# Performance work log

Hardware: AMD Instinct MI355X
Metric: run time of the kernel (lower is better)

The kernel has to match this reference:

```python
import jax, jax.numpy as jnp
import numpy as np

S = 197      # 'attention_heads' arg, acts as sequence length
D = 768      # embedding_dim
H = 4 * D    # MLP hidden
B = 64
EPS = 1e-5
SCALE = 1.0 / S ** (-0.5)  # faithful to source: equals sqrt(S)


def _ln(x, w, b):
    # LayerNorm over the last two dims (S, D), elementwise affine (S, D)
    mu = jnp.mean(x, axis=(-2, -1), keepdims=True)
    var = jnp.var(x, axis=(-2, -1), keepdims=True)
    return (x - mu) * jax.lax.rsqrt(var + EPS) * w + b


def setup_inputs() -> dict:
    key = jax.random.key(0)
    ks = jax.random.split(key, 16)
    s = 0.02
    return {
        "x": jax.random.normal(ks[0], (B, S, D), jnp.float32),
        "norm1_w": jnp.ones((S, D), jnp.float32),
        "norm1_b": jnp.zeros((S, D), jnp.float32),
        "Wq": jax.random.normal(ks[1], (D, D), jnp.float32) * s,
        "bq": jnp.zeros((D,), jnp.float32),
        "Wk": jax.random.normal(ks[2], (D, D), jnp.float32) * s,
        "bk": jnp.zeros((D,), jnp.float32),
        "Wv": jax.random.normal(ks[3], (D, D), jnp.float32) * s,
        "bv": jnp.zeros((D,), jnp.float32),
        "norm2_w": jnp.ones((S, D), jnp.float32),
        "norm2_b": jnp.zeros((S, D), jnp.float32),
        "W1": jax.random.normal(ks[4], (D, H), jnp.float32) * s,
        "b1": jnp.zeros((H,), jnp.float32),
        "W2": jax.random.normal(ks[5], (H, D), jnp.float32) * s,
        "b2": jnp.zeros((D,), jnp.float32),
    }


def reference(x, norm1_w, norm1_b, Wq, bq, Wk, bk, Wv, bv,
              norm2_w, norm2_b, W1, b1, W2, b2):
    # --- attention block ---
    h = _ln(x, norm1_w, norm1_b)                     # (B, S, D)
    q = jnp.einsum('bsd,de->bse', h, Wq) + bq
    k = jnp.einsum('bsd,de->bse', h, Wk) + bk
    v = jnp.einsum('bsd,de->bse', h, Wv) + bv
    scores = jnp.einsum('bsd,btd->bst', q, k) * SCALE  # (B, S, S)
    attn = jnp.einsum('bst,btd->bsd', jax.nn.softmax(scores, axis=-1), v)
    x = attn + x
    # --- MLP block ---
    h2 = _ln(x, norm2_w, norm2_b)
    hid = jax.nn.gelu(jnp.einsum('bsd,dh->bsh', h2, W1) + b1, approximate=False)
    mlp = jax.nn.gelu(jnp.einsum('bsh,hd->bsd', hid, W2) + b2, approximate=False)
    return mlp + x
```

## Files before the change

### kernel.cpp

```cpp
#include <hip/hip_runtime.h>
#include <math.h>


#define S_LEN 197
#define DIM   768
#define HDIM  3072
#define BATCH 64
#define NT    (BATCH * S_LEN)
#define NTP   12672
#define SD    (S_LEN * DIM)
#define SROWS 208
#define SCOLS 224
#define PROWS 256

typedef __attribute__((ext_vector_type(4))) float  f32x4;
typedef __attribute__((ext_vector_type(8))) short  short8v;
typedef __attribute__((ext_vector_type(4))) short  short4v;
typedef __attribute__((ext_vector_type(4))) unsigned short ushort4v;

__device__ __forceinline__ ushort f2bf(float f) {
  union { float f; unsigned u; } a; a.f = f;
  unsigned u = a.u;
  u += 0x7FFFu + ((u >> 16) & 1u);
  return (ushort)(u >> 16);
}
__device__ __forceinline__ float b2f(ushort h) {
  union { unsigned u; float f; } a; a.u = ((unsigned)h) << 16;
  return a.f;
}
__device__ __forceinline__ float gelu_f(float x) {
  return 0.5f * x * (1.0f + erff(x * 0.7071067811865476f));
}
__device__ __forceinline__ void gload16(const void* g, void* l) {
  __builtin_amdgcn_global_load_lds(
      (const __attribute__((address_space(1))) void*)g,
      (__attribute__((address_space(3))) void*)l, 16, 0, 0);
}

template<bool SPLIT>
__global__ __launch_bounds__(256) void transp_k(const float* __restrict__ W,
                                                int K, int N,
                                                ushort* __restrict__ Thi,
                                                ushort* __restrict__ Tlo) {
  __shared__ float tile[32][33];
  const int nb = blockIdx.x * 32, kb = blockIdx.y * 32;
  const int tx = threadIdx.x, ty = threadIdx.y;
#pragma unroll
  for (int i = 0; i < 4; ++i)
    tile[ty + i * 8][tx] = W[(size_t)(kb + ty + i * 8) * N + nb + tx];
  __syncthreads();
#pragma unroll
  for (int i = 0; i < 4; ++i) {
    float v = tile[tx][ty + i * 8];
    size_t o = (size_t)(nb + ty + i * 8) * K + kb + tx;
    ushort h = f2bf(v);
    Thi[o] = h;
    if (SPLIT) Tlo[o] = f2bf(v - b2f(h));
  }
}

#define LN_CH 4
__global__ __launch_bounds__(256) void ln_part_k(const float* __restrict__ x,
                                                 float* __restrict__ pbuf) {
  const int c = blockIdx.x, b = blockIdx.y;
  const float4* xv = (const float4*)(x + (size_t)b * SD);
  const int per = (SD / 4) / LN_CH;
  float sum = 0.f, sq = 0.f;
  for (int i = c * per + threadIdx.x; i < (c + 1) * per; i += 256) {
    float4 v = xv[i];
    sum += (v.x + v.y) + (v.z + v.w);
    sq  += (v.x * v.x + v.y * v.y) + (v.z * v.z + v.w * v.w);
  }
#pragma unroll
  for (int o = 32; o > 0; o >>= 1) {
    sum += __shfl_xor(sum, o); sq += __shfl_xor(sq, o);
  }
  __shared__ float s1[4], s2[4];
  if ((threadIdx.x & 63) == 0) { s1[threadIdx.x >> 6] = sum; s2[threadIdx.x >> 6] = sq; }
  __syncthreads();
  if (threadIdx.x == 0) {
    pbuf[(b * LN_CH + c) * 2]     = s1[0] + s1[1] + s1[2] + s1[3];
    pbuf[(b * LN_CH + c) * 2 + 1] = s2[0] + s2[1] + s2[2] + s2[3];
  }
}

__global__ __launch_bounds__(64) void ln_fin_k(const float* __restrict__ pbuf,
                                               float* __restrict__ stats) {
  const int b = threadIdx.x;
  float S = 0.f, Q = 0.f;
#pragma unroll
  for (int c = 0; c < LN_CH; ++c) {
    S += pbuf[(b * LN_CH + c) * 2];
    Q += pbuf[(b * LN_CH + c) * 2 + 1];
  }
  const float mu = S / (float)SD;
  const float var = Q / (float)SD - mu * mu;
  stats[b * 2] = mu;
  stats[b * 2 + 1] = 1.0f / sqrtf(var + 1e-5f);
}

template<bool SPLIT>
__global__ __launch_bounds__(256) void ln_apply_k(const float* __restrict__ x,
                                                  const float* __restrict__ w,
                                                  const float* __restrict__ bb,
                                                  const float* __restrict__ stats,
                                                  ushort* __restrict__ oHi,
                                                  ushort* __restrict__ oLo) {
  const int b = blockIdx.y;
  const int i = blockIdx.x * 256 + threadIdx.x;
  if (i >= SD / 4) return;
  const float mu = stats[b * 2], rs = stats[b * 2 + 1];
  float4 v  = ((const float4*)(x + (size_t)b * SD))[i];
  float4 W4 = ((const float4*)w)[i];
  float4 B4 = ((const float4*)bb)[i];
  float h0 = (v.x - mu) * rs * W4.x + B4.x;
  float h1 = (v.y - mu) * rs * W4.y + B4.y;
  float h2 = (v.z - mu) * rs * W4.z + B4.z;
  float h3 = (v.w - mu) * rs * W4.w + B4.w;
  ushort4v hh;
  hh[0] = f2bf(h0); hh[1] = f2bf(h1); hh[2] = f2bf(h2); hh[3] = f2bf(h3);
  ((ushort4v*)(oHi + (size_t)b * SD))[i] = hh;
  if (SPLIT) {
    ushort4v ll;
    ll[0] = f2bf(h0 - b2f(hh[0]));
    ll[1] = f2bf(h1 - b2f(hh[1]));
    ll[2] = f2bf(h2 - b2f(hh[2]));
    ll[3] = f2bf(h3 - b2f(hh[3]));
    ((ushort4v*)(oLo + (size_t)b * SD))[i] = ll;
  }
}

__global__ __launch_bounds__(64) void softmax_k(const float* __restrict__ scores,
                                                ushort* __restrict__ P) {
  const int s = blockIdx.x, b = blockIdx.y;
  const int lane = threadIdx.x;
  const float* row = scores + ((size_t)b * SROWS + s) * SCOLS;
  float v[4];
  float m = -1e30f;
#pragma unroll
  for (int t = 0; t < 4; ++t) {
    int c = lane + t * 64;
    v[t] = (c < S_LEN) ? row[c] : -1e30f;
    m = fmaxf(m, v[t]);
  }
#pragma unroll
  for (int off = 32; off > 0; off >>= 1) m = fmaxf(m, __shfl_xor(m, off));
  float sum = 0.f;
#pragma unroll
  for (int t = 0; t < 4; ++t) {
    int c = lane + t * 64;
    v[t] = (c < S_LEN) ? expf(v[t] - m) : 0.f;
    sum += v[t];
  }
#pragma unroll
  for (int off = 32; off > 0; off >>= 1) sum += __shfl_xor(sum, off);
  const float inv = 1.0f / sum;
  ushort* prow = P + ((size_t)b * PROWS + s) * SCOLS;
#pragma unroll
  for (int t = 0; t < 4; ++t) {
    int c = lane + t * 64;
    if (c < SCOLS) prow[c] = f2bf(v[t] * inv);
  }
}

#define GBM 128
#define GBN 128

enum { EPI_QK = 0, EPI_V, EPI_SCORE, EPI_PV, EPI_GELU, EPI_OUT };

struct GemmArgs {
  const ushort* Ahi; const ushort* Alo; size_t sAb; int lda;
  const ushort* Bhi; const ushort* Blo; size_t sBb; int ldb;
  int K; int Mv; int Nv;
  const float* bias;
  const float* resid; size_t sRb; int ldr;
  float scale;
  float* outF; size_t sOb; int ldo;
  ushort* outHi; ushort* outLo;
};

template<int BK>
__device__ __forceinline__ short8v frag_ld(const ushort* tile, int row, int cb) {
  constexpr int SMASK = (BK * 2) / 16 - 1;
  const char* base = (const char*)tile + row * (BK * 2);
  const int xr = (row & SMASK) << 4;
  const int c1 = cb + 32;
  union U { short8v v8; struct P4 { short4v a, b; } p4; } f;
  f.p4.a = *(const short4v*)(base + ((( cb & ~15) ^ xr) | (cb & 15)));
  f.p4.b = *(const short4v*)(base + (((c1 & ~15) ^ xr) | (c1 & 15)));
  return f.v8;
}

__device__ __forceinline__ short8v load_frag(const ushort* p) {
  union U { short8v v8; struct P4 { short4v a, b; } p4; } f;
  f.p4.a = *(const short4v*)(p);
  f.p4.b = *(const short4v*)(p + 16);
  return f.v8;
}

template<int NPROD, bool TRANSB, int EPI, int BK>
__global__ __launch_bounds__(256) void gemm_k(GemmArgs g) {
  constexpr int KSH2 = (BK == 64) ? 7 : 6;
  constexpr int SMASK = (BK * 2) / 16 - 1;
  constexpr int ASZ  = GBM * BK;
  constexpr int BSTR = TRANSB ? 44 : BK;
  constexpr int BSZ  = GBN * BSTR;
  __shared__ __align__(16) ushort sm[(NPROD == 3) ? (2 * ASZ + 2 * BSZ)
                                                  : (ASZ + BSZ)];
  ushort* sAhi = sm;
  ushort* sBhi = sm + ASZ;
  ushort* sAlo = sm + ASZ + BSZ;
  ushort* sBlo = sm + 2 * ASZ + BSZ;

  const int tid  = threadIdx.x;
  const int lane = tid & 63;
  const int wid  = tid >> 6;
  const int r    = lane & 15;
  const int gg   = lane >> 4;
  const int wrow = wid >> 1;
  const int wcol = wid & 1;

  const int gx = gridDim.x, gy = gridDim.y;
  const int nwg = gx * gy;
  const int orig = blockIdx.x + gx * blockIdx.y;
  const int qq = nwg >> 3, rr = nwg & 7;
  const int xcd = orig & 7, idx = orig >> 3;
  const int wg = (xcd < rr ? xcd * (qq + 1) : rr * (qq + 1) + (xcd - rr) * qq) + idx;
  const int nbase = (wg % gx) * GBN;
  const int mbase = (wg / gx) * GBM;
  const int b     = blockIdx.z;

  const ushort* Ahi = g.Ahi + (size_t)b * g.sAb;
  const ushort* Bhi = g.Bhi + (size_t)b * g.sBb;
  const ushort* Alo = (NPROD == 3) ? (g.Alo + (size_t)b * g.sAb) : (const ushort*)nullptr;
  const ushort* Blo = (NPROD == 3) ? (g.Blo + (size_t)b * g.sBb) : (const ushort*)nullptr;

  f32x4 acc[4][4];
#pragma unroll
  for (int i = 0; i < 4; ++i)
#pragma unroll
    for (int j = 0; j < 4; ++j) {
      acc[i][j][0] = 0.f; acc[i][j][1] = 0.f; acc[i][j][2] = 0.f; acc[i][j][3] = 0.f;
    }

  const int wvb = wid << 10;

  for (int kk = 0; kk < g.K; kk += BK) {
    __syncthreads();
#pragma unroll
    for (int rd = 0; rd < BK / 16; ++rd) {
      const int boff = rd * 4096 + tid * 16;
      const int row  = boff >> KSH2;
      const int slot = (boff >> 4) & SMASK;
      const int scol = ((slot ^ (row & SMASK)) << 3);
      const size_t gaoff = (size_t)(mbase + row) * g.lda + (kk + scol);
      gload16(Ahi + gaoff, (char*)sAhi + rd * 4096 + wvb);
      if (NPROD == 3)
        gload16(Alo + gaoff, (char*)sAlo + rd * 4096 + wvb);
      if (!TRANSB) {
        const size_t gboff = (size_t)(nbase + row) * g.ldb + (kk + scol);
        gload16(Bhi + gboff, (char*)sBhi + rd * 4096 + wvb);
        if (NPROD == 3)
          gload16(Blo + gboff, (char*)sBlo + rd * 4096 + wvb);
      }
    }
    if (TRANSB) {
#pragma unroll
      for (int rd = 0; rd < (BK * 128) / 2048; ++rd) {
        const int lin = tid * 8 + rd * 2048;
        const int kr = lin >> 7, nc = lin & 127;
        union { short8v v; ushort u[8]; } t;
        t.v = *(const short8v*)(Bhi + (size_t)(kk + kr) * g.ldb + (nbase + nc));
#pragma unroll
        for (int e = 0; e < 8; ++e)
          sBhi[(nc + e) * BSTR + kr] = t.u[e];
      }
    }
    __syncthreads();

#pragma unroll
    for (int kb = 0; kb < BK / 32; ++kb) {
      const int cbk = kb * 64 + gg * 8;
      short8v aH[4], bH[4], aL[4], bL[4];
#pragma unroll
      for (int i = 0; i < 4; ++i) {
        const int arow = wrow * 64 + i * 16 + r;
        aH[i] = frag_ld<BK>(sAhi, arow, cbk);
        if (NPROD == 3) aL[i] = frag_ld<BK>(sAlo, arow, cbk);
      }
#pragma unroll
      for (int j = 0; j < 4; ++j) {
        const int brow = wcol * 64 + j * 16 + r;
        if (!TRANSB) {
          bH[j] = frag_ld<BK>(sBhi, brow, cbk);
          if (NPROD == 3) bL[j] = frag_ld<BK>(sBlo, brow, cbk);
        } else {
          bH[j] = load_frag(sBhi + brow * BSTR + kb * 32 + gg * 4);
        }
      }
#pragma unroll
      for (int i = 0; i < 4; ++i)
#pragma unroll
        for (int j = 0; j < 4; ++j) {
          acc[i][j] = __builtin_amdgcn_mfma_f32_16x16x32_bf16(aH[i], bH[j], acc[i][j], 0, 0, 0);
          if (NPROD == 3) {
            acc[i][j] = __builtin_amdgcn_mfma_f32_16x16x32_bf16(aH[i], bL[j], acc[i][j], 0, 0, 0);
            acc[i][j] = __builtin_amdgcn_mfma_f32_16x16x32_bf16(aL[i], bH[j], acc[i][j], 0, 0, 0);
          }
        }
    }
  }

#pragma unroll
  for (int i = 0; i < 4; ++i)
#pragma unroll
    for (int j = 0; j < 4; ++j)
#pragma unroll
      for (int e = 0; e < 4; ++e) {
        const int row = mbase + wrow * 64 + i * 16 + gg * 4 + e;
        const int col = nbase + wcol * 64 + j * 16 + r;
        float val = acc[i][j][e];
        if (EPI == EPI_QK) {
          val += g.bias[col];
          ushort hi = f2bf(val);
          ushort lo = f2bf(val - b2f(hi));
          size_t o = (size_t)row * g.ldo + col;
          g.outHi[o] = hi; g.outLo[o] = lo;
        } else if (EPI == EPI_V) {
          val += g.bias[col];
          g.outHi[(size_t)row * g.ldo + col] = f2bf(val);
        } else if (EPI == EPI_SCORE) {
          if (row < g.Mv && col < g.Nv)
            (g.outF + (size_t)b * g.sOb)[(size_t)row * g.ldo + col] = val * g.scale;
        } else if (EPI == EPI_PV) {
          if (row < g.Mv) {
            val += (g.resid + (size_t)b * g.sRb)[(size_t)row * g.ldr + col];
            (g.outF + (size_t)b * g.sOb)[(size_t)row * g.ldo + col] = val;
          }
        } else if (EPI == EPI_GELU) {
          val = gelu_f(val + g.bias[col]);
          g.outHi[(size_t)row * g.ldo + col] = f2bf(val);
        } else {
          if (row < g.Mv) {
            val = gelu_f(val + g.bias[col]);
            val += g.resid[(size_t)row * g.ldr + col];
            g.outF[(size_t)row * g.ldo + col] = val;
          }
        }
      }
}

extern "C" void kernel_launch(void* const* d_in, const int* in_sizes, int n_in,
                              void* d_out, int out_size, void* d_ws, size_t ws_size,
                              hipStream_t stream) {
  const float* x   = (const float*)d_in[0];
  const float* n1w = (const float*)d_in[1];
  const float* n1b = (const float*)d_in[2];
  const float* Wq  = (const float*)d_in[3];
  const float* bq  = (const float*)d_in[4];
  const float* Wk  = (const float*)d_in[5];
  const float* bk  = (const float*)d_in[6];
  const float* Wv  = (const float*)d_in[7];
  const float* bv  = (const float*)d_in[8];
  const float* n2w = (const float*)d_in[9];
  const float* n2b = (const float*)d_in[10];
  const float* W1  = (const float*)d_in[11];
  const float* b1  = (const float*)d_in[12];
  const float* W2  = (const float*)d_in[13];
  const float* b2  = (const float*)d_in[14];
  float* out = (float*)d_out;

  char* ws = (char*)d_ws;
  size_t off = 0;
  auto alloc = [&](size_t bytes) -> char* {
    char* p = ws + off;
    off += (bytes + 255) & ~(size_t)255;
    return p;
  };
  const size_t szDD  = (size_t)DIM * DIM * 2;
  const size_t szDH  = (size_t)DIM * HDIM * 2;
  const size_t szAct = (size_t)NTP * DIM * 2;

  ushort* wqtH = (ushort*)alloc(szDD);
  ushort* wqtL = (ushort*)alloc(szDD);
  ushort* wktH = (ushort*)alloc(szDD);
  ushort* wktL = (ushort*)alloc(szDD);
  ushort* wvtH = (ushort*)alloc(szDD);
  ushort* w1tH = (ushort*)alloc(szDH);
  ushort* w2tH = (ushort*)alloc(szDH);
  ushort* hHi  = (ushort*)alloc(szAct);
  ushort* hLo  = (ushort*)alloc(szAct);
  ushort* qHi  = (ushort*)alloc(szAct);
  ushort* qLo  = (ushort*)alloc(szAct);
  ushort* kHi  = (ushort*)alloc(szAct);
  ushort* kLo  = (ushort*)alloc(szAct);
  ushort* vB   = (ushort*)alloc(szAct);
  float*  scoresWs = (float*)alloc((size_t)BATCH * SROWS * SCOLS * 4);
  ushort* pWs      = (ushort*)alloc((size_t)BATCH * PROWS * SCOLS * 2);
  float*  lnPart   = (float*)alloc((size_t)BATCH * LN_CH * 2 * 4);
  float*  lnStats  = (float*)alloc((size_t)BATCH * 2 * 4);
  if (off > ws_size) return;

  float*  x2  = (float*)hHi;
  ushort* h2  = vB;
  ushort* hid = qHi;

  const float SCALE_F = 14.035668847618199f;

  dim3 tb(32, 8);
  hipLaunchKernelGGL((transp_k<true >), dim3(DIM / 32, DIM / 32), tb, 0, stream, Wq, DIM, DIM, wqtH, wqtL);
  hipLaunchKernelGGL((transp_k<true >), dim3(DIM / 32, DIM / 32), tb, 0, stream, Wk, DIM, DIM, wktH, wktL);
  hipLaunchKernelGGL((transp_k<false>), dim3(DIM / 32, DIM / 32), tb, 0, stream, Wv, DIM, DIM, wvtH, (ushort*)nullptr);
  hipLaunchKernelGGL((transp_k<false>), dim3(HDIM / 32, DIM / 32), tb, 0, stream, W1, DIM, HDIM, w1tH, (ushort*)nullptr);
  hipLaunchKernelGGL((transp_k<false>), dim3(DIM / 32, HDIM / 32), tb, 0, stream, W2, HDIM, DIM, w2tH, (ushort*)nullptr);

  const int APPLY_BX = (SD / 4 + 255) / 256;
  hipLaunchKernelGGL(ln_part_k, dim3(LN_CH, BATCH), dim3(256), 0, stream, x, lnPart);
  hipLaunchKernelGGL(ln_fin_k, dim3(1), dim3(64), 0, stream, lnPart, lnStats);
  hipLaunchKernelGGL((ln_apply_k<true>), dim3(APPLY_BX, BATCH), dim3(256), 0, stream,
                     x, n1w, n1b, lnStats, hHi, hLo);

  GemmArgs a;
  const int BIG = 0x40000000;

  a = GemmArgs{};
  a.Ahi = hHi; a.Alo = hLo; a.sAb = 0; a.lda = DIM;
  a.Bhi = wqtH; a.Blo = wqtL; a.sBb = 0; a.ldb = DIM;
  a.K = DIM; a.Mv = BIG; a.Nv = BIG; a.bias = bq; a.scale = 1.f;
  a.outHi = qHi; a.outLo = qLo; a.ldo = DIM;
  hipLaunchKernelGGL((gemm_k<3, false, EPI_QK, 32>), dim3(DIM / GBN, NTP / GBM, 1), dim3(256), 0, stream, a);
  a.Bhi = wktH; a.Blo = wktL; a.bias = bk; a.outHi = kHi; a.outLo = kLo;
  hipLaunchKernelGGL((gemm_k<3, false, EPI_QK, 32>), dim3(DIM / GBN, NTP / GBM, 1), dim3(256), 0, stream, a);
  a = GemmArgs{};
  a.Ahi = hHi; a.sAb = 0; a.lda = DIM;
  a.Bhi = wvtH; a.sBb = 0; a.ldb = DIM;
  a.K = DIM; a.Mv = BIG; a.Nv = BIG; a.bias = bv;
  a.outHi = vB; a.ldo = DIM;
  hipLaunchKernelGGL((gemm_k<1, false, EPI_V, 64>), dim3(DIM / GBN, NTP / GBM, 1), dim3(256), 0, stream, a);

  a = GemmArgs{};
  a.Ahi = qHi; a.Alo = qLo; a.sAb = (size_t)SD; a.lda = DIM;
  a.Bhi = kHi; a.Blo = kLo; a.sBb = (size_t)SD; a.ldb = DIM;
  a.K = DIM; a.Mv = S_LEN; a.Nv = S_LEN; a.scale = SCALE_F;
  a.outF = scoresWs; a.sOb = (size_t)SROWS * SCOLS; a.ldo = SCOLS;
  hipLaunchKernelGGL((gemm_k<3, false, EPI_SCORE, 32>), dim3(2, 2, BATCH), dim3(256), 0, stream, a);

  hipLaunchKernelGGL(softmax_k, dim3(S_LEN, BATCH), dim3(64), 0, stream, scoresWs, pWs);

  a = GemmArgs{};
  a.Ahi = pWs; a.sAb = (size_t)PROWS * SCOLS; a.lda = SCOLS;
  a.Bhi = vB; a.sBb = (size_t)SD; a.ldb = DIM;
  a.K = SCOLS; a.Mv = S_LEN; a.Nv = BIG;
  a.resid = x; a.sRb = (size_t)SD; a.ldr = DIM;
  a.outF = x2; a.sOb = (size_t)SD; a.ldo = DIM;
  hipLaunchKernelGGL((gemm_k<1, true, EPI_PV, 32>), dim3(DIM / GBN, 2, BATCH), dim3(256), 0, stream, a);

  hipLaunchKernelGGL(ln_part_k, dim3(LN_CH, BATCH), dim3(256), 0, stream, x2, lnPart);
  hipLaunchKernelGGL(ln_fin_k, dim3(1), dim3(64), 0, stream, lnPart, lnStats);
  hipLaunchKernelGGL((ln_apply_k<false>), dim3(APPLY_BX, BATCH), dim3(256), 0, stream,
                     x2, n2w, n2b, lnStats, h2, (ushort*)nullptr);

  a = GemmArgs{};
  a.Ahi = h2; a.sAb = 0; a.lda = DIM;
  a.Bhi = w1tH; a.sBb = 0; a.ldb = DIM;
  a.K = DIM; a.Mv = BIG; a.Nv = BIG; a.bias = b1;
  a.outHi = hid; a.ldo = HDIM;
  hipLaunchKernelGGL((gemm_k<1, false, EPI_GELU, 64>), dim3(HDIM / GBN, NTP / GBM, 1), dim3(256), 0, stream, a);

  a = GemmArgs{};
  a.Ahi = hid; a.sAb = 0; a.lda = HDIM;
  a.Bhi = w2tH; a.sBb = 0; a.ldb = HDIM;
  a.K = HDIM; a.Mv = NT; a.Nv = BIG; a.bias = b2;
  a.resid = x2; a.sRb = 0; a.ldr = DIM;
  a.outF = out; a.sOb = 0; a.ldo = DIM;
  hipLaunchKernelGGL((gemm_k<1, false, EPI_OUT, 64>), dim3(DIM / GBN, NTP / GBM, 1), dim3(256), 0, stream, a);
}
```

Before: 937.2 us.

## Double-buffer GEMM LDS staging and switch GELU to tanh approximation

For non-transposed-B GEMMs, the shared memory tile becomes double-buffered so the async global-to-LDS loads for the next K step are issued before computing on the current one, with one barrier per iteration. This is meant to overlap memory latency with MFMA work, at the cost of twice the LDS footprint and possibly lower occupancy. Separately, the exact erf GELU is replaced by the tanh approximation built on __expf. That removes the cost of erff but departs from the reference, which requires exact GELU (approximate=False).

```diff
diff --git a/kernel.cpp b/kernel.cpp
--- a/kernel.cpp
+++ b/kernel.cpp
@@ -29,7 +29,11 @@
   return a.f;
 }
 __device__ __forceinline__ float gelu_f(float x) {
-  return 0.5f * x * (1.0f + erff(x * 0.7071067811865476f));
+  float x3 = x * x * x;
+  float y2 = 1.5957691216057308f * (x + 0.044715f * x3);
+  float e  = __expf(y2);
+  float t  = 1.0f - 2.0f / (e + 1.0f);
+  return 0.5f * x * (1.0f + t);
 }
 __device__ __forceinline__ void gload16(const void* g, void* l) {
   __builtin_amdgcn_global_load_lds(
@@ -205,12 +209,8 @@
   constexpr int ASZ  = GBM * BK;
   constexpr int BSTR = TRANSB ? 44 : BK;
   constexpr int BSZ  = GBN * BSTR;
-  __shared__ __align__(16) ushort sm[(NPROD == 3) ? (2 * ASZ + 2 * BSZ)
-                                                  : (ASZ + BSZ)];
-  ushort* sAhi = sm;
-  ushort* sBhi = sm + ASZ;
-  ushort* sAlo = sm + ASZ + BSZ;
-  ushort* sBlo = sm + 2 * ASZ + BSZ;
+  constexpr int BUFSZ = (NPROD == 3) ? (2 * ASZ + 2 * BSZ) : (ASZ + BSZ);
+  __shared__ __align__(16) ushort sm[TRANSB ? (ASZ + BSZ) : 2 * BUFSZ];
 
   const int tid  = threadIdx.x;
   const int lane = tid & 63;
@@ -245,8 +245,11 @@
 
   const int wvb = wid << 10;
 
-  for (int kk = 0; kk < g.K; kk += BK) {
-    __syncthreads();
+  auto STAGE = [&](int kk, ushort* base) {
+    ushort* dA  = base;
+    ushort* dB  = base + ASZ;
+    ushort* dAl = base + ASZ + BSZ;
+    ushort* dBl = base + 2 * ASZ + BSZ;
 #pragma unroll
     for (int rd = 0; rd < BK / 16; ++rd) {
       const int boff = rd * 4096 + tid * 16;
@@ -254,30 +257,21 @@
       const int slot = (boff >> 4) & SMASK;
       const int scol = ((slot ^ (row & SMASK)) << 3);
       const size_t gaoff = (size_t)(mbase + row) * g.lda + (kk + scol);
-      gload16(Ahi + gaoff, (char*)sAhi + rd * 4096 + wvb);
+      gload16(Ahi + gaoff, (char*)dA + rd * 4096 + wvb);
       if (NPROD == 3)
-        gload16(Alo + gaoff, (char*)sAlo + rd * 4096 + wvb);
-      if (!TRANSB) {
-        const size_t gboff = (size_t)(nbase + row) * g.ldb + (kk + scol);
-        gload16(Bhi + gboff, (char*)sBhi + rd * 4096 + wvb);
-        if (NPROD == 3)
-          gload16(Blo + gboff, (char*)sBlo + rd * 4096 + wvb);
-      }
+        gload16(Alo + gaoff, (char*)dAl + rd * 4096 + wvb);
+      const size_t gboff = (size_t)(nbase + row) * g.ldb + (kk + scol);
+      gload16(Bhi + gboff, (char*)dB + rd * 4096 + wvb);
+      if (NPROD == 3)
+        gload16(Blo + gboff, (char*)dBl + rd * 4096 + wvb);
     }
-    if (TRANSB) {
-#pragma unroll
-      for (int rd = 0; rd < (BK * 128) / 2048; ++rd) {
-        const int lin = tid * 8 + rd * 2048;
-        const int kr = lin >> 7, nc = lin & 127;
-        union { short8v v; ushort u[8]; } t;
-        t.v = *(const short8v*)(Bhi + (size_t)(kk + kr) * g.ldb + (nbase + nc));
-#pragma unroll
-        for (int e = 0; e < 8; ++e)
-          sBhi[(nc + e) * BSTR + kr] = t.u[e];
-      }
-    }
-    __syncthreads();
-
+  };
+
+  auto COMPUTE = [&](const ushort* base) {
+    const ushort* cA  = base;
+    const ushort* cB  = base + ASZ;
+    const ushort* cAl = base + ASZ + BSZ;
+    const ushort* cBl = base + 2 * ASZ + BSZ;
 #pragma unroll
     for (int kb = 0; kb < BK / 32; ++kb) {
       const int cbk = kb * 64 + gg * 8;
@@ -285,18 +279,14 @@
 #pragma unroll
       for (int i = 0; i < 4; ++i) {
         const int arow = wrow * 64 + i * 16 + r;
-        aH[i] = frag_ld<BK>(sAhi, arow, cbk);
-        if (NPROD == 3) aL[i] = frag_ld<BK>(sAlo, arow, cbk);
+        aH[i] = frag_ld<BK>(cA, arow, cbk);
+        if (NPROD == 3) aL[i] = frag_ld<BK>(cAl, arow, cbk);
       }
 #pragma unroll
       for (int j = 0; j < 4; ++j) {
         const int brow = wcol * 64 + j * 16 + r;
-        if (!TRANSB) {
-          bH[j] = frag_ld<BK>(sBhi, brow, cbk);
-          if (NPROD == 3) bL[j] = frag_ld<BK>(sBlo, brow, cbk);
-        } else {
-          bH[j] = load_frag(sBhi + brow * BSTR + kb * 32 + gg * 4);
-        }
+        bH[j] = frag_ld<BK>(cB, brow, cbk);
+        if (NPROD == 3) bL[j] = frag_ld<BK>(cBl, brow, cbk);
       }
 #pragma unroll
       for (int i = 0; i < 4; ++i)
@@ -308,6 +298,61 @@
             acc[i][j] = __builtin_amdgcn_mfma_f32_16x16x32_bf16(aL[i], bH[j], acc[i][j], 0, 0, 0);
           }
         }
+    }
+  };
+
+  if (!TRANSB) {
+    STAGE(0, sm);
+    __syncthreads();
+    const int nst = g.K / BK;
+    for (int t = 0; t < nst; ++t) {
+      ushort* cur = sm + (t & 1) * BUFSZ;
+      ushort* nxt = sm + ((t & 1) ^ 1) * BUFSZ;
+      if (t + 1 < nst) STAGE((t + 1) * BK, nxt);
+      COMPUTE(cur);
+      if (t + 1 < nst) __syncthreads();
+    }
+  } else {
+    ushort* sAhi = sm;
+    ushort* sBhi = sm + ASZ;
+    for (int kk = 0; kk < g.K; kk += BK) {
+      __syncthreads();
+#pragma unroll
+      for (int rd = 0; rd < BK / 16; ++rd) {
+        const int boff = rd * 4096 + tid * 16;
+        const int row  = boff >> KSH2;
+        const int slot = (boff >> 4) & SMASK;
+        const int scol = ((slot ^ (row & SMASK)) << 3);
+        const size_t gaoff = (size_t)(mbase + row) * g.lda + (kk + scol);
+        gload16(Ahi + gaoff, (char*)sAhi + rd * 4096 + wvb);
+      }
+#pragma unroll
+      for (int rd = 0; rd < (BK * 128) / 2048; ++rd) {
+        const int lin = tid * 8 + rd * 2048;
+        const int kr = lin >> 7, nc = lin & 127;
+        union { short8v v; ushort u[8]; } t;
+        t.v = *(const short8v*)(Bhi + (size_t)(kk + kr) * g.ldb + (nbase + nc));
+#pragma unroll
+        for (int e = 0; e < 8; ++e)
+          sBhi[(nc + e) * BSTR + kr] = t.u[e];
+      }
+      __syncthreads();
+#pragma unroll
+      for (int kb = 0; kb < BK / 32; ++kb) {
+        const int cbk = kb * 64 + gg * 8;
+        short8v aH[4], bH[4];
+#pragma unroll
+        for (int i = 0; i < 4; ++i)
+          aH[i] = frag_ld<BK>(sAhi, wrow * 64 + i * 16 + r, cbk);
+#pragma unroll
+        for (int j = 0; j < 4; ++j)
+          bH[j] = load_frag(sBhi + (wcol * 64 + j * 16 + r) * BSTR + kb * 32 + gg * 4);
+#pragma unroll
+        for (int i = 0; i < 4; ++i)
+#pragma unroll
+          for (int j = 0; j < 4; ++j)
+            acc[i][j] = __builtin_amdgcn_mfma_f32_16x16x32_bf16(aH[i], bH[j], acc[i][j], 0, 0, 0);
+      }
     }
   }
 
```

New measurement: 753.3 us. 19.6% less time.
